# Kernel optimization log

Hardware: AMD Instinct MI355X
Metric: run time of the kernel (lower is better)

## Reference

```python
import jax, jax.numpy as jnp
import numpy as np

D_MODEL = 256; N_LAYERS = 4; INPUT_LEN = 15
D_INNER = 512; D_STATE = 16; D_CONV = 4; DT_RANK = 16
BATCH = 4; SEQ = 2048; EPS = 1e-5

def _ln(x, w, b):
    m = jnp.mean(x, -1, keepdims=True)
    v = jnp.var(x, -1, keepdims=True)
    return (x - m) * jax.lax.rsqrt(v + EPS) * w + b

def _silu(x):
    return x * jax.nn.sigmoid(x)

def _mixer(h, inW, cw, cb, xpW, dtW, dtb, A_log, Dp, opW):
    # h: [B,L,d_model]
    xz = h @ inW.T                      # [B,L,2*D_INNER]
    xh, z = jnp.split(xz, 2, axis=-1)
    # causal depthwise conv1d
    xc = jnp.transpose(xh, (0, 2, 1))   # [B,D,L]
    xc = jax.lax.conv_general_dilated(xc, cw, (1,), [(D_CONV - 1, 0)],
                                      feature_group_count=D_INNER,
                                      dimension_numbers=('NCH', 'OIH', 'NCH'))
    xc = xc + cb[None, :, None]
    xh = _silu(jnp.transpose(xc, (0, 2, 1)))  # [B,L,D]
    dbl = xh @ xpW.T                    # [B,L,DT_RANK+2N]
    dt = dbl[..., :DT_RANK]
    Bm = dbl[..., DT_RANK:DT_RANK + D_STATE]
    C = dbl[..., DT_RANK + D_STATE:]
    dt = jax.nn.softplus(dt @ dtW.T + dtb)    # [B,L,D]
    A = -jnp.exp(A_log)                       # [D,N]
    dA = jnp.exp(dt[..., None] * A)           # [B,L,D,N]
    dBu = dt[..., None] * Bm[:, :, None, :] * xh[..., None]  # [B,L,D,N]
    def step(hst, inp):
        dA_t, dBu_t, C_t = inp
        hst = dA_t * hst + dBu_t
        y = jnp.einsum('bdn,bn->bd', hst, C_t)
        return hst, y
    h0 = jnp.zeros((xh.shape[0], D_INNER, D_STATE), xh.dtype)
    _, ys = jax.lax.scan(step, h0, (jnp.transpose(dA, (1, 0, 2, 3)),
                                    jnp.transpose(dBu, (1, 0, 2, 3)),
                                    jnp.transpose(C, (1, 0, 2))))
    y = jnp.transpose(ys, (1, 0, 2)) + Dp * xh
    y = y * _silu(z)
    return y @ opW.T

def setup_inputs():
    key = jax.random.key(0)
    ks = jax.random.split(key, 8)
    s = 0.02
    return {
        'x_src': jax.random.normal(ks[0], (BATCH, SEQ, INPUT_LEN), jnp.float32),
        'single_eval_pos': 1024,
        'in_W': jax.random.normal(ks[1], (D_MODEL, INPUT_LEN)) * s,
        'norm_w': jnp.ones((N_LAYERS, D_MODEL)),
        'norm_b': jnp.zeros((N_LAYERS, D_MODEL)),
        'inproj_W': jax.random.normal(ks[2], (N_LAYERS, 2 * D_INNER, D_MODEL)) * s,
        'conv_w': jax.random.normal(ks[3], (N_LAYERS, D_INNER, 1, D_CONV)) * 0.2,
        'conv_b': jnp.zeros((N_LAYERS, D_INNER)),
        'xproj_W': jax.random.normal(ks[4], (N_LAYERS, DT_RANK + 2 * D_STATE, D_INNER)) * s,
        'dtproj_W': jax.random.normal(ks[5], (N_LAYERS, D_INNER, DT_RANK)) * 0.1,
        'dtproj_b': jnp.log(jnp.expm1(jnp.full((N_LAYERS, D_INNER), 0.01))),
        'A_log': jnp.log(jnp.broadcast_to(jnp.arange(1, D_STATE + 1, dtype=jnp.float32), (N_LAYERS, D_INNER, D_STATE)) + 0.0),
        'D_param': jnp.ones((N_LAYERS, D_INNER)),
        'outproj_W': jax.random.normal(ks[6], (N_LAYERS, D_MODEL, D_INNER)) * s,
        'out_W': jax.random.normal(ks[7], (1, D_MODEL)) * s,
    }

def reference(x_src, single_eval_pos, in_W, norm_w, norm_b, inproj_W, conv_w, conv_b, xproj_W, dtproj_W, dtproj_b, A_log, D_param, outproj_W, out_W):
    h = x_src @ in_W.T                  # [B,L,d_model]
    res = None
    for i in range(N_LAYERS):
        res = h if res is None else h + res
        hn = _ln(res, norm_w[i], norm_b[i])
        h = _mixer(hn, inproj_W[i], conv_w[i], conv_b[i], xproj_W[i],
                   dtproj_W[i], dtproj_b[i], A_log[i], D_param[i], outproj_W[i])
    # backbone returns hidden_states directly (norm_f defined but not applied)
    return h @ out_W.T                  # [B,L,1]
```

## Files before the change

### kernel.cpp

```cpp
#include <hip/hip_runtime.h>

#define B_   4
#define T_   2048
#define BT_  8192
#define INL  15
#define DM   256
#define DI   512
#define DX   1024
#define DS_  16
#define DR_  16
#define NO_  48
#define NL   4
#define NC_  128
#define LCH  16

typedef short bf16x8 __attribute__((ext_vector_type(8)));
typedef float f32x4  __attribute__((ext_vector_type(4)));

__device__ __forceinline__ float sigmoidf_(float x){ return 1.f/(1.f+__expf(-x)); }

__device__ __forceinline__ unsigned short f2bf(float x){
    union { float f; unsigned u; } v; v.f = x;
    unsigned r = (v.u + 0x7FFFu + ((v.u >> 16) & 1u)) >> 16;
    return (unsigned short)r;
}
__device__ __forceinline__ float bf2f(unsigned short h){
    union { unsigned u; float f; } v; v.u = ((unsigned)h) << 16;
    return v.f;
}

__device__ __forceinline__ void ld16(const float* __restrict__ p, float* v){
    const float4* q = (const float4*)p;
    float4 x0=q[0],x1=q[1],x2=q[2],x3=q[3];
    v[0]=x0.x; v[1]=x0.y; v[2]=x0.z; v[3]=x0.w;
    v[4]=x1.x; v[5]=x1.y; v[6]=x1.z; v[7]=x1.w;
    v[8]=x2.x; v[9]=x2.y; v[10]=x2.z; v[11]=x2.w;
    v[12]=x3.x; v[13]=x3.y; v[14]=x3.z; v[15]=x3.w;
}
__device__ __forceinline__ void st16(float* __restrict__ p, const float* v){
    float4* q = (float4*)p;
    q[0] = make_float4(v[0],v[1],v[2],v[3]);
    q[1] = make_float4(v[4],v[5],v[6],v[7]);
    q[2] = make_float4(v[8],v[9],v[10],v[11]);
    q[3] = make_float4(v[12],v[13],v[14],v[15]);
}

__global__ void k_cvtW(const float* __restrict__ W, unsigned short* __restrict__ hi,
                       unsigned short* __restrict__ lo, int n4){
    int g = blockIdx.x*256 + threadIdx.x;
    if(g >= n4) return;
    float4 v = ((const float4*)W)[g];
    ushort4 h, l;
    h.x = f2bf(v.x); l.x = f2bf(v.x - bf2f(h.x));
    h.y = f2bf(v.y); l.y = f2bf(v.y - bf2f(h.y));
    h.z = f2bf(v.z); l.z = f2bf(v.z - bf2f(h.z));
    h.w = f2bf(v.w); l.w = f2bf(v.w - bf2f(h.w));
    ((ushort4*)hi)[g] = h;
    ((ushort4*)lo)[g] = l;
}

__global__ void k_ingemm(const float* __restrict__ x, const float* __restrict__ W,
                         float* __restrict__ h){
    int g  = blockIdx.x*256 + threadIdx.x;
    int bt = g >> 8, m = g & 255;
    const float* xr = x + bt*INL;
    const float* wr = W + m*INL;
    float acc = 0.f;
#pragma unroll
    for(int k=0;k<INL;k++) acc += xr[k]*wr[k];
    h[g] = acc;
}

__global__ void k_resln(const float* __restrict__ h, float* __restrict__ res,
                        unsigned short* __restrict__ hnhi, unsigned short* __restrict__ hnlo,
                        const float* __restrict__ w, const float* __restrict__ b, int addRes){
    int wv = threadIdx.x >> 6, lane = threadIdx.x & 63;
    int bt = blockIdx.x*4 + wv;
    float4 v = ((const float4*)(h + (size_t)bt*DM))[lane];
    if(addRes){
        float4 r = ((const float4*)(res + (size_t)bt*DM))[lane];
        v.x+=r.x; v.y+=r.y; v.z+=r.z; v.w+=r.w;
    }
    ((float4*)(res + (size_t)bt*DM))[lane] = v;
    float s  = v.x+v.y+v.z+v.w;
    float ss = v.x*v.x+v.y*v.y+v.z*v.z+v.w*v.w;
#pragma unroll
    for(int m=1;m<64;m<<=1){ s += __shfl_xor(s,m); ss += __shfl_xor(ss,m); }
    float mean = s*(1.f/DM);
    float var  = ss*(1.f/DM) - mean*mean;
    float inv  = rsqrtf(var + 1e-5f);
    float4 wt = ((const float4*)w)[lane];
    float4 bs = ((const float4*)b)[lane];
    float4 o;
    o.x = (v.x-mean)*inv*wt.x + bs.x;
    o.y = (v.y-mean)*inv*wt.y + bs.y;
    o.z = (v.z-mean)*inv*wt.z + bs.z;
    o.w = (v.w-mean)*inv*wt.w + bs.w;
    ushort4 hh, ll;
    hh.x = f2bf(o.x); ll.x = f2bf(o.x - bf2f(hh.x));
    hh.y = f2bf(o.y); ll.y = f2bf(o.y - bf2f(hh.y));
    hh.z = f2bf(o.z); ll.z = f2bf(o.z - bf2f(hh.z));
    hh.w = f2bf(o.w); ll.w = f2bf(o.w - bf2f(hh.w));
    ((ushort4*)(hnhi + (size_t)bt*DM))[lane] = hh;
    ((ushort4*)(hnlo + (size_t)bt*DM))[lane] = ll;
}

template<int BM,int BN>
__global__ void __launch_bounds__(256) k_gemm_bf3(
    const unsigned short* __restrict__ Ahi, const unsigned short* __restrict__ Alo,
    const unsigned short* __restrict__ Bhi, const unsigned short* __restrict__ Blo,
    float* __restrict__ C, int M, int N, int K)
{
    constexpr int LDP = 40;
    constexpr int WM = BM/2, WN = BN/2;
    constexpr int MI_ = WM/16, NI_ = WN/16;
    __shared__ unsigned short sAh[BM*LDP], sAl[BM*LDP], sBh[BN*LDP], sBl[BN*LDP];
    int tid  = threadIdx.x;
    int wave = tid >> 6, lane = tid & 63;
    int wm0  = (wave >> 1) * WM, wn0 = (wave & 1) * WN;
    int m0   = blockIdx.y * BM, n0 = blockIdx.x * BN;
    int lr   = lane & 15;
    int kq   = (lane >> 4) * 8;
    int quad4 = (lane >> 4) * 4;

    f32x4 acc[MI_][NI_];
#pragma unroll
    for(int i=0;i<MI_;i++)
#pragma unroll
        for(int j=0;j<NI_;j++) acc[i][j] = (f32x4){0.f,0.f,0.f,0.f};

    for(int k0=0;k0<K;k0+=32){
#pragma unroll
        for(int i=tid;i<BM*4;i+=256){
            int r = i>>2, cg = (i&3)*8;
            size_t go = (size_t)(m0+r)*K + k0 + cg;
            *(float4*)(&sAh[r*LDP + cg]) = *(const float4*)(Ahi + go);
            *(float4*)(&sAl[r*LDP + cg]) = *(const float4*)(Alo + go);
        }
#pragma unroll
        for(int i=tid;i<BN*4;i+=256){
            int r = i>>2, cg = (i&3)*8;
            size_t go = (size_t)(n0+r)*K + k0 + cg;
            *(float4*)(&sBh[r*LDP + cg]) = *(const float4*)(Bhi + go);
            *(float4*)(&sBl[r*LDP + cg]) = *(const float4*)(Blo + go);
        }
        __syncthreads();
        bf16x8 ah[MI_], al[MI_], bh[NI_], bl[NI_];
#pragma unroll
        for(int mi=0;mi<MI_;mi++){
            int ro = (wm0 + mi*16 + lr)*LDP + kq;
            ah[mi] = *(const bf16x8*)(&sAh[ro]);
            al[mi] = *(const bf16x8*)(&sAl[ro]);
        }
#pragma unroll
        for(int ni=0;ni<NI_;ni++){
            int ro = (wn0 + ni*16 + lr)*LDP + kq;
            bh[ni] = *(const bf16x8*)(&sBh[ro]);
            bl[ni] = *(const bf16x8*)(&sBl[ro]);
        }
#pragma unroll
        for(int mi=0;mi<MI_;mi++)
#pragma unroll
            for(int ni=0;ni<NI_;ni++){
                acc[mi][ni] = __builtin_amdgcn_mfma_f32_16x16x32_bf16(ah[mi], bh[ni], acc[mi][ni], 0,0,0);
                acc[mi][ni] = __builtin_amdgcn_mfma_f32_16x16x32_bf16(ah[mi], bl[ni], acc[mi][ni], 0,0,0);
                acc[mi][ni] = __builtin_amdgcn_mfma_f32_16x16x32_bf16(al[mi], bh[ni], acc[mi][ni], 0,0,0);
            }
        __syncthreads();
    }
#pragma unroll
    for(int mi=0;mi<MI_;mi++)
#pragma unroll
        for(int ni=0;ni<NI_;ni++){
            int col = n0 + wn0 + ni*16 + lr;
#pragma unroll
            for(int r=0;r<4;r++){
                int row = m0 + wm0 + mi*16 + quad4 + r;
                C[(size_t)row*N + col] = acc[mi][ni][r];
            }
        }
}

__global__ void __launch_bounds__(512) k_convxp(
    const float* __restrict__ xz, const float* __restrict__ cw, const float* __restrict__ cb,
    const unsigned short* __restrict__ Bhi, const unsigned short* __restrict__ Blo,
    const float* __restrict__ dtW, const float* __restrict__ dtbias,
    const float* __restrict__ A_log,
    float* __restrict__ xh, float* __restrict__ bc, float* __restrict__ dtO,
    float* __restrict__ S, float* __restrict__ sdt)
{
    __shared__ unsigned short sAh[16*520], sAl[16*520];
    __shared__ float sbc[16*36];
    __shared__ float dls[16*17];

    int tid = threadIdx.x;
    int wave = tid >> 6, lane = tid & 63;
    int lr = lane & 15, kq = (lane>>4)*8, quad4 = (lane>>4)*4;
    int m0 = blockIdx.x * LCH;
    int d  = tid;

    float xv[19];
    {
        int rbase = m0 - 3;
        bool mask0 = ((m0 & (T_-1)) == 0);
#pragma unroll
        for(int j=0;j<19;j++)
            xv[j] = (mask0 && j<3) ? 0.f : xz[(size_t)(rbase+j)*DX + d];
    }
    float4 w4 = *(const float4*)(cw + d*4);
    float bias = cb[d];
    float xhreg[16];
#pragma unroll
    for(int t=0;t<16;t++){
        float a = bias + w4.x*xv[t] + w4.y*xv[t+1] + w4.z*xv[t+2] + w4.w*xv[t+3];
        float v = a * sigmoidf_(a);
        xhreg[t] = v;
        xh[(size_t)(m0+t)*DI + d] = v;
        unsigned short hh = f2bf(v);
        sAh[t*520 + d] = hh;
        sAl[t*520 + d] = f2bf(v - bf2f(hh));
    }
    float wr_[16]; ld16(dtW + (size_t)d*16, wr_);
    float a_[16];  ld16(A_log + (size_t)d*16, a_);
#pragma unroll
    for(int n=0;n<16;n++) a_[n] = -__expf(a_[n]);
    float bsv = dtbias[d];
    __syncthreads();

    f32x4 acc = {0.f,0.f,0.f,0.f};
    if(wave < 3){
#pragma unroll 4
        for(int ks=0;ks<16;ks++){
            int ao = lr*520 + ks*32 + kq;
            bf16x8 ah = *(const bf16x8*)(&sAh[ao]);
            bf16x8 al = *(const bf16x8*)(&sAl[ao]);
            size_t wo = (size_t)(wave*16 + lr)*DI + ks*32 + kq;
            bf16x8 bh = *(const bf16x8*)(Bhi + wo);
            bf16x8 bl = *(const bf16x8*)(Blo + wo);
            acc = __builtin_amdgcn_mfma_f32_16x16x32_bf16(ah, bh, acc, 0,0,0);
            acc = __builtin_amdgcn_mfma_f32_16x16x32_bf16(ah, bl, acc, 0,0,0);
            acc = __builtin_amdgcn_mfma_f32_16x16x32_bf16(al, bh, acc, 0,0,0);
        }
        if(wave == 0){
#pragma unroll
            for(int r=0;r<4;r++) dls[(quad4+r)*17 + lr] = acc[r];
        } else if(wave == 1){
#pragma unroll
            for(int r=0;r<4;r++){
                sbc[(quad4+r)*36 + lr] = acc[r];
                bc[(size_t)(m0+quad4+r)*32 + lr] = acc[r];
            }
        } else {
#pragma unroll
            for(int r=0;r<4;r++){
                sbc[(quad4+r)*36 + 16 + lr] = acc[r];
                bc[(size_t)(m0+quad4+r)*32 + 16 + lr] = acc[r];
            }
        }
    }
    __syncthreads();

    float dtreg[16];
#pragma unroll
    for(int t=0;t<16;t++){
        float acc2 = bsv;
#pragma unroll
        for(int r=0;r<16;r++) acc2 += dls[t*17 + r]*wr_[r];
        float sp = fmaxf(acc2,0.f) + log1pf(__expf(-fabsf(acc2)));
        dtreg[t] = sp;
        dtO[(size_t)(m0+t)*DI + d] = sp;
    }
    float st_[16];
#pragma unroll
    for(int n=0;n<16;n++) st_[n] = 0.f;
    float sd = 0.f;
#pragma unroll 4
    for(int t=0;t<16;t++){
        float dtv = dtreg[t];
        float dx  = dtv*xhreg[t];
        sd += dtv;
        float bv[16]; ld16(&sbc[t*36], bv);
#pragma unroll
        for(int n=0;n<16;n++) st_[n] = __expf(dtv*a_[n])*st_[n] + dx*bv[n];
    }
    int b = m0 >> 11, c = (m0 >> 4) & (NC_-1);
    st16(S + (((size_t)b*NC_ + c)*DI + d)*16, st_);
    sdt[((size_t)b*NC_ + c)*DI + d] = sd;
}

__global__ void k_scan2(const float* __restrict__ S, const float* __restrict__ sdt,
                        const float* __restrict__ A_log, float* __restrict__ Hinit){
    int g = blockIdx.x*256 + threadIdx.x;
    int b = g >> 13;
    int dn = g & 8191;
    int d = dn >> 4;
    float a = -__expf(A_log[dn]);
    float H = 0.f;
    for(int c=0;c<NC_;c++){
        size_t o = ((size_t)(b*NC_ + c))*8192 + dn;
        Hinit[o] = H;
        float sd = sdt[(size_t)(b*NC_ + c)*DI + d];
        H = __expf(sd*a)*H + S[o];
    }
}

__global__ void __launch_bounds__(512) k_scan3o(
    const float* __restrict__ dt, const float* __restrict__ xh, const float* __restrict__ xz,
    const float* __restrict__ bc, const float* __restrict__ A_log, const float* __restrict__ Dpar,
    const float* __restrict__ Hinit, const unsigned short* __restrict__ Whi,
    const unsigned short* __restrict__ Wlo, float* __restrict__ hOut)
{
    __shared__ unsigned short sYh[16*540], sYl[16*540];
    __shared__ float sbc[16*36];
    int tid = threadIdx.x;
    int c = blockIdx.x, b = blockIdx.y;
    int m0 = b*T_ + c*LCH;
    if(tid < 128){
        int t = tid >> 3, s = tid & 7;
        *(float4*)(&sbc[t*36 + s*4]) = *(const float4*)(bc + (size_t)(m0+t)*32 + s*4);
    }
    __syncthreads();
    {
        int d = tid;
        float a_[16]; ld16(A_log + (size_t)d*16, a_);
#pragma unroll
        for(int n=0;n<16;n++) a_[n] = -__expf(a_[n]);
        float st_[16]; ld16(Hinit + (((size_t)b*NC_ + c)*DI + d)*16, st_);
        float Dp = Dpar[d];
#pragma unroll 4
        for(int t=0;t<LCH;t++){
            int bt = m0 + t;
            float dtv = dt[(size_t)bt*DI + d];
            float xhv = xh[(size_t)bt*DI + d];
            float bv[16]; ld16(&sbc[t*36], bv);
            float cv[16]; ld16(&sbc[t*36 + 16], cv);
            float dx = dtv*xhv;
            float y = 0.f;
#pragma unroll
            for(int n=0;n<16;n++){
                st_[n] = __expf(dtv*a_[n])*st_[n] + dx*bv[n];
                y += st_[n]*cv[n];
            }
            float zv = xz[(size_t)bt*DX + DI + d];
            y += Dp*xhv;
            y = y * zv * sigmoidf_(zv);
            unsigned short hh = f2bf(y);
            sYh[t*540 + d] = hh;
            sYl[t*540 + d] = f2bf(y - bf2f(hh));
        }
    }
    __syncthreads();
    int wave = tid >> 6, lane = tid & 63;
    int lr = lane & 15, kq = (lane>>4)*8, quad4 = (lane>>4)*4;
    f32x4 acc[2];
    acc[0] = (f32x4){0.f,0.f,0.f,0.f};
    acc[1] = (f32x4){0.f,0.f,0.f,0.f};
#pragma unroll 4
    for(int ks=0;ks<16;ks++){
        int ao = lr*540 + ks*32 + kq;
        bf16x8 ah = *(const bf16x8*)(&sYh[ao]);
        bf16x8 al = *(const bf16x8*)(&sYl[ao]);
#pragma unroll
        for(int nj=0;nj<2;nj++){
            int n = (wave*2 + nj)*16 + lr;
            size_t wo = (size_t)n*DI + ks*32 + kq;
            bf16x8 bh = *(const bf16x8*)(Whi + wo);
            bf16x8 bl = *(const bf16x8*)(Wlo + wo);
            acc[nj] = __builtin_amdgcn_mfma_f32_16x16x32_bf16(ah, bh, acc[nj], 0,0,0);
            acc[nj] = __builtin_amdgcn_mfma_f32_16x16x32_bf16(ah, bl, acc[nj], 0,0,0);
            acc[nj] = __builtin_amdgcn_mfma_f32_16x16x32_bf16(al, bh, acc[nj], 0,0,0);
        }
    }
#pragma unroll
    for(int nj=0;nj<2;nj++){
        int col = (wave*2 + nj)*16 + lr;
#pragma unroll
        for(int r=0;r<4;r++){
            int row = m0 + quad4 + r;
            hOut[(size_t)row*DM + col] = acc[nj][r];
        }
    }
}

__global__ void k_outw(const float* __restrict__ h, const float* __restrict__ ow,
                       float* __restrict__ out){
    int wv = threadIdx.x >> 6, lane = threadIdx.x & 63;
    int bt = blockIdx.x*4 + wv;
    float4 v = ((const float4*)(h + (size_t)bt*DM))[lane];
    float4 w = ((const float4*)ow)[lane];
    float s = v.x*w.x + v.y*w.y + v.z*w.z + v.w*w.w;
#pragma unroll
    for(int m=1;m<64;m<<=1) s += __shfl_xor(s,m);
    if(lane==0) out[bt] = s;
}

extern "C" void kernel_launch(void* const* d_in, const int* in_sizes, int n_in,
                              void* d_out, int out_size, void* d_ws, size_t ws_size,
                              hipStream_t stream){
    const float* x_src    = (const float*)d_in[0];
    const float* in_W     = (const float*)d_in[2];
    const float* norm_w   = (const float*)d_in[3];
    const float* norm_b   = (const float*)d_in[4];
    const float* inproj_W = (const float*)d_in[5];
    const float* conv_w   = (const float*)d_in[6];
    const float* conv_b   = (const float*)d_in[7];
    const float* xproj_W  = (const float*)d_in[8];
    const float* dtproj_W = (const float*)d_in[9];
    const float* dtproj_b = (const float*)d_in[10];
    const float* A_log    = (const float*)d_in[11];
    const float* D_param  = (const float*)d_in[12];
    const float* outproj_W= (const float*)d_in[13];
    const float* out_W    = (const float*)d_in[14];

    float* ws  = (float*)d_ws;
    float* h    = ws;
    float* res  = h    + (size_t)BT_*DM;
    float* xz   = res  + (size_t)BT_*DM;
    float* xh   = xz   + (size_t)BT_*DX;
    float* bcb  = xh   + (size_t)BT_*DI;
    float* dtb  = bcb  + (size_t)BT_*32;
    float* sdtb = dtb  + (size_t)BT_*DI;
    float* Sbuf = sdtb + (size_t)B_*NC_*DI;
    float* Hbuf = Sbuf + (size_t)B_*NC_*DI*DS_;
    unsigned short* us = (unsigned short*)(Hbuf + (size_t)B_*NC_*DI*DS_);
    unsigned short* WhiIn  = us;
    unsigned short* WloIn  = WhiIn  + (size_t)NL*DX*DM;
    unsigned short* WhiOut = WloIn  + (size_t)NL*DX*DM;
    unsigned short* WloOut = WhiOut + (size_t)NL*DM*DI;
    unsigned short* WhiXp  = WloOut + (size_t)NL*DM*DI;
    unsigned short* WloXp  = WhiXp  + (size_t)NL*NO_*DI;
    unsigned short* hnhi   = WloXp  + (size_t)NL*NO_*DI;
    unsigned short* hnlo   = hnhi   + (size_t)BT_*DM;

    k_cvtW<<<(NL*DX*DM/4 + 255)/256, 256, 0, stream>>>(inproj_W,  WhiIn,  WloIn,  NL*DX*DM/4);
    k_cvtW<<<(NL*DM*DI/4 + 255)/256, 256, 0, stream>>>(outproj_W, WhiOut, WloOut, NL*DM*DI/4);
    k_cvtW<<<(NL*NO_*DI/4 + 255)/256, 256, 0, stream>>>(xproj_W, WhiXp, WloXp, NL*NO_*DI/4);
    k_ingemm<<<BT_*DM/256, 256, 0, stream>>>(x_src, in_W, h);
    for(int i=0;i<NL;i++){
        k_resln<<<BT_/4, 256, 0, stream>>>(h, res, hnhi, hnlo, norm_w + i*DM, norm_b + i*DM, i>0 ? 1 : 0);
        k_gemm_bf3<128,128><<<dim3(DX/128, BT_/128), 256, 0, stream>>>(
            hnhi, hnlo, WhiIn + (size_t)i*DX*DM, WloIn + (size_t)i*DX*DM, xz, BT_, DX, DM);
        k_convxp<<<BT_/LCH, 512, 0, stream>>>(xz, conv_w + i*DI*4, conv_b + i*DI,
            WhiXp + (size_t)i*NO_*DI, WloXp + (size_t)i*NO_*DI,
            dtproj_W + (size_t)i*DI*DR_, dtproj_b + i*DI, A_log + (size_t)i*DI*DS_,
            xh, bcb, dtb, Sbuf, sdtb);
        k_scan2<<<B_*DI*DS_/256, 256, 0, stream>>>(Sbuf, sdtb, A_log + (size_t)i*DI*DS_, Hbuf);
        k_scan3o<<<dim3(NC_, B_), 512, 0, stream>>>(dtb, xh, xz, bcb, A_log + (size_t)i*DI*DS_,
            D_param + i*DI, Hbuf, WhiOut + (size_t)i*DM*DI, WloOut + (size_t)i*DM*DI, h);
    }
    k_outw<<<BT_/4, 256, 0, stream>>>(h, out_W, (float*)d_out);
}
```

Before: 627.8 us.

## Split out-projection into tiled GEMM fused with residual add and layernorm

The scan kernel no longer computes the out-projection. It writes packed hi/lo bf16 outputs to a buffer instead. A new 64-row tiled MFMA kernel stages the out-projection weights in shared memory, reusing them across 64 rows rather than reloading them from global memory for every 16-row chunk. The same kernel fuses the residual add and the next layer's layernorm, which removes the separate resln launch for layers after the first. The cost is an extra round trip of the Y buffer through global memory and one more kernel launch per layer.

```diff
diff --git a/kernel.cpp b/kernel.cpp
--- a/kernel.cpp
+++ b/kernel.cpp
@@ -304,13 +304,11 @@
     }
 }
 
-__global__ void __launch_bounds__(512) k_scan3o(
+__global__ void __launch_bounds__(512) k_scan3(
     const float* __restrict__ dt, const float* __restrict__ xh, const float* __restrict__ xz,
     const float* __restrict__ bc, const float* __restrict__ A_log, const float* __restrict__ Dpar,
-    const float* __restrict__ Hinit, const unsigned short* __restrict__ Whi,
-    const unsigned short* __restrict__ Wlo, float* __restrict__ hOut)
+    const float* __restrict__ Hinit, unsigned* __restrict__ Y)
 {
-    __shared__ unsigned short sYh[16*540], sYl[16*540];
     __shared__ float sbc[16*36];
     int tid = threadIdx.x;
     int c = blockIdx.x, b = blockIdx.y;
@@ -320,65 +318,152 @@
         *(float4*)(&sbc[t*36 + s*4]) = *(const float4*)(bc + (size_t)(m0+t)*32 + s*4);
     }
     __syncthreads();
-    {
-        int d = tid;
-        float a_[16]; ld16(A_log + (size_t)d*16, a_);
-#pragma unroll
-        for(int n=0;n<16;n++) a_[n] = -__expf(a_[n]);
-        float st_[16]; ld16(Hinit + (((size_t)b*NC_ + c)*DI + d)*16, st_);
-        float Dp = Dpar[d];
+    int d = tid;
+    float a_[16]; ld16(A_log + (size_t)d*16, a_);
+#pragma unroll
+    for(int n=0;n<16;n++) a_[n] = -__expf(a_[n]);
+    float st_[16]; ld16(Hinit + (((size_t)b*NC_ + c)*DI + d)*16, st_);
+    float Dp = Dpar[d];
 #pragma unroll 4
-        for(int t=0;t<LCH;t++){
-            int bt = m0 + t;
-            float dtv = dt[(size_t)bt*DI + d];
-            float xhv = xh[(size_t)bt*DI + d];
-            float bv[16]; ld16(&sbc[t*36], bv);
-            float cv[16]; ld16(&sbc[t*36 + 16], cv);
-            float dx = dtv*xhv;
-            float y = 0.f;
-#pragma unroll
-            for(int n=0;n<16;n++){
-                st_[n] = __expf(dtv*a_[n])*st_[n] + dx*bv[n];
-                y += st_[n]*cv[n];
+    for(int t=0;t<LCH;t++){
+        int bt = m0 + t;
+        float dtv = dt[(size_t)bt*DI + d];
+        float xhv = xh[(size_t)bt*DI + d];
+        float bv[16]; ld16(&sbc[t*36], bv);
+        float cv[16]; ld16(&sbc[t*36 + 16], cv);
+        float dx = dtv*xhv;
+        float y = 0.f;
+#pragma unroll
+        for(int n=0;n<16;n++){
+            st_[n] = __expf(dtv*a_[n])*st_[n] + dx*bv[n];
+            y += st_[n]*cv[n];
+        }
+        float zv = xz[(size_t)bt*DX + DI + d];
+        y += Dp*xhv;
+        y = y * zv * sigmoidf_(zv);
+        unsigned short hh = f2bf(y);
+        unsigned short ll = f2bf(y - bf2f(hh));
+        Y[(size_t)bt*DI + d] = (unsigned)hh | ((unsigned)ll << 16);
+    }
+}
+
+__global__ void __launch_bounds__(256) k_outln(
+    const unsigned* __restrict__ Y, const unsigned short* __restrict__ Bhi,
+    const unsigned short* __restrict__ Blo, float* __restrict__ res,
+    const float* __restrict__ nw, const float* __restrict__ nb,
+    unsigned short* __restrict__ hnhi, unsigned short* __restrict__ hnlo,
+    float* __restrict__ hOut, int last)
+{
+    __shared__ __align__(16) char smem[66560];
+    unsigned short* sAh = (unsigned short*)smem;
+    unsigned short* sAl = sAh + 64*40;
+    unsigned short* sBh = sAl + 64*40;
+    unsigned short* sBl = sBh + 256*40;
+    float* sC = (float*)smem;
+
+    int tid = threadIdx.x;
+    int wave = tid >> 6, lane = tid & 63;
+    int wm0 = (wave >> 1)*32, wn0 = (wave & 1)*128;
+    int m0 = blockIdx.x*64;
+    int lr = lane & 15, kq = (lane>>4)*8, quad4 = (lane>>4)*4;
+
+    f32x4 acc[2][8];
+#pragma unroll
+    for(int i=0;i<2;i++)
+#pragma unroll
+        for(int j=0;j<8;j++) acc[i][j] = (f32x4){0.f,0.f,0.f,0.f};
+
+    for(int k0=0;k0<DI;k0+=32){
+        {
+            int r = tid>>2, s = tid&3;
+            const uint4* yp = (const uint4*)(Y + (size_t)(m0+r)*DI + k0 + s*8);
+            uint4 p0 = yp[0], p1 = yp[1];
+            union { bf16x8 v; unsigned short u[8]; } H, L;
+            H.u[0]=(unsigned short)p0.x; L.u[0]=(unsigned short)(p0.x>>16);
+            H.u[1]=(unsigned short)p0.y; L.u[1]=(unsigned short)(p0.y>>16);
+            H.u[2]=(unsigned short)p0.z; L.u[2]=(unsigned short)(p0.z>>16);
+            H.u[3]=(unsigned short)p0.w; L.u[3]=(unsigned short)(p0.w>>16);
+            H.u[4]=(unsigned short)p1.x; L.u[4]=(unsigned short)(p1.x>>16);
+            H.u[5]=(unsigned short)p1.y; L.u[5]=(unsigned short)(p1.y>>16);
+            H.u[6]=(unsigned short)p1.z; L.u[6]=(unsigned short)(p1.z>>16);
+            H.u[7]=(unsigned short)p1.w; L.u[7]=(unsigned short)(p1.w>>16);
+            *(bf16x8*)(&sAh[r*40 + s*8]) = H.v;
+            *(bf16x8*)(&sAl[r*40 + s*8]) = L.v;
+        }
+#pragma unroll
+        for(int i=tid;i<1024;i+=256){
+            int r = i>>2, s = i&3;
+            size_t go = (size_t)r*DI + k0 + s*8;
+            *(float4*)(&sBh[r*40 + s*8]) = *(const float4*)(Bhi + go);
+            *(float4*)(&sBl[r*40 + s*8]) = *(const float4*)(Blo + go);
+        }
+        __syncthreads();
+        bf16x8 ah[2], al[2];
+#pragma unroll
+        for(int mi=0;mi<2;mi++){
+            int ro = (wm0 + mi*16 + lr)*40 + kq;
+            ah[mi] = *(const bf16x8*)(&sAh[ro]);
+            al[mi] = *(const bf16x8*)(&sAl[ro]);
+        }
+#pragma unroll
+        for(int ni=0;ni<8;ni++){
+            int ro = (wn0 + ni*16 + lr)*40 + kq;
+            bf16x8 bh = *(const bf16x8*)(&sBh[ro]);
+            bf16x8 bl = *(const bf16x8*)(&sBl[ro]);
+#pragma unroll
+            for(int mi=0;mi<2;mi++){
+                acc[mi][ni] = __builtin_amdgcn_mfma_f32_16x16x32_bf16(ah[mi], bh, acc[mi][ni], 0,0,0);
+                acc[mi][ni] = __builtin_amdgcn_mfma_f32_16x16x32_bf16(ah[mi], bl, acc[mi][ni], 0,0,0);
+                acc[mi][ni] = __builtin_amdgcn_mfma_f32_16x16x32_bf16(al[mi], bh, acc[mi][ni], 0,0,0);
             }
-            float zv = xz[(size_t)bt*DX + DI + d];
-            y += Dp*xhv;
-            y = y * zv * sigmoidf_(zv);
-            unsigned short hh = f2bf(y);
-            sYh[t*540 + d] = hh;
-            sYl[t*540 + d] = f2bf(y - bf2f(hh));
-        }
-    }
+        }
+        __syncthreads();
+    }
+#pragma unroll
+    for(int mi=0;mi<2;mi++)
+#pragma unroll
+        for(int ni=0;ni<8;ni++){
+            int col = wn0 + ni*16 + lr;
+#pragma unroll
+            for(int r=0;r<4;r++)
+                sC[(wm0 + mi*16 + quad4 + r)*260 + col] = acc[mi][ni][r];
+        }
     __syncthreads();
-    int wave = tid >> 6, lane = tid & 63;
-    int lr = lane & 15, kq = (lane>>4)*8, quad4 = (lane>>4)*4;
-    f32x4 acc[2];
-    acc[0] = (f32x4){0.f,0.f,0.f,0.f};
-    acc[1] = (f32x4){0.f,0.f,0.f,0.f};
-#pragma unroll 4
-    for(int ks=0;ks<16;ks++){
-        int ao = lr*540 + ks*32 + kq;
-        bf16x8 ah = *(const bf16x8*)(&sYh[ao]);
-        bf16x8 al = *(const bf16x8*)(&sYl[ao]);
-#pragma unroll
-        for(int nj=0;nj<2;nj++){
-            int n = (wave*2 + nj)*16 + lr;
-            size_t wo = (size_t)n*DI + ks*32 + kq;
-            bf16x8 bh = *(const bf16x8*)(Whi + wo);
-            bf16x8 bl = *(const bf16x8*)(Wlo + wo);
-            acc[nj] = __builtin_amdgcn_mfma_f32_16x16x32_bf16(ah, bh, acc[nj], 0,0,0);
-            acc[nj] = __builtin_amdgcn_mfma_f32_16x16x32_bf16(ah, bl, acc[nj], 0,0,0);
-            acc[nj] = __builtin_amdgcn_mfma_f32_16x16x32_bf16(al, bh, acc[nj], 0,0,0);
-        }
-    }
-#pragma unroll
-    for(int nj=0;nj<2;nj++){
-        int col = (wave*2 + nj)*16 + lr;
-#pragma unroll
-        for(int r=0;r<4;r++){
-            int row = m0 + quad4 + r;
-            hOut[(size_t)row*DM + col] = acc[nj][r];
-        }
+    float4 wt, bs;
+    if(!last){
+        wt = ((const float4*)nw)[lane];
+        bs = ((const float4*)nb)[lane];
+    }
+    for(int j=0;j<16;j++){
+        int row = wave*16 + j;
+        int gr  = m0 + row;
+        float4 cv = *(float4*)(&sC[row*260 + lane*4]);
+        if(last){
+            ((float4*)(hOut + (size_t)gr*DM))[lane] = cv;
+            continue;
+        }
+        float4 rv = ((const float4*)(res + (size_t)gr*DM))[lane];
+        cv.x+=rv.x; cv.y+=rv.y; cv.z+=rv.z; cv.w+=rv.w;
+        ((float4*)(res + (size_t)gr*DM))[lane] = cv;
+        float s  = cv.x+cv.y+cv.z+cv.w;
+        float ss = cv.x*cv.x+cv.y*cv.y+cv.z*cv.z+cv.w*cv.w;
+#pragma unroll
+        for(int m=1;m<64;m<<=1){ s += __shfl_xor(s,m); ss += __shfl_xor(ss,m); }
+        float mean = s*(1.f/DM);
+        float var  = ss*(1.f/DM) - mean*mean;
+        float inv  = rsqrtf(var + 1e-5f);
+        float4 o;
+        o.x = (cv.x-mean)*inv*wt.x + bs.x;
+        o.y = (cv.y-mean)*inv*wt.y + bs.y;
+        o.z = (cv.z-mean)*inv*wt.z + bs.z;
+        o.w = (cv.w-mean)*inv*wt.w + bs.w;
+        ushort4 hh, ll;
+        hh.x = f2bf(o.x); ll.x = f2bf(o.x - bf2f(hh.x));
+        hh.y = f2bf(o.y); ll.y = f2bf(o.y - bf2f(hh.y));
+        hh.z = f2bf(o.z); ll.z = f2bf(o.z - bf2f(hh.z));
+        hh.w = f2bf(o.w); ll.w = f2bf(o.w - bf2f(hh.w));
+        ((ushort4*)(hnhi + (size_t)gr*DM))[lane] = hh;
+        ((ushort4*)(hnlo + (size_t)gr*DM))[lane] = ll;
     }
 }
 
@@ -431,13 +516,14 @@
     unsigned short* WloXp  = WhiXp  + (size_t)NL*NO_*DI;
     unsigned short* hnhi   = WloXp  + (size_t)NL*NO_*DI;
     unsigned short* hnlo   = hnhi   + (size_t)BT_*DM;
+    unsigned*       ybuf   = (unsigned*)(hnlo + (size_t)BT_*DM);
 
     k_cvtW<<<(NL*DX*DM/4 + 255)/256, 256, 0, stream>>>(inproj_W,  WhiIn,  WloIn,  NL*DX*DM/4);
     k_cvtW<<<(NL*DM*DI/4 + 255)/256, 256, 0, stream>>>(outproj_W, WhiOut, WloOut, NL*DM*DI/4);
     k_cvtW<<<(NL*NO_*DI/4 + 255)/256, 256, 0, stream>>>(xproj_W, WhiXp, WloXp, NL*NO_*DI/4);
     k_ingemm<<<BT_*DM/256, 256, 0, stream>>>(x_src, in_W, h);
+    k_resln<<<BT_/4, 256, 0, stream>>>(h, res, hnhi, hnlo, norm_w, norm_b, 0);
     for(int i=0;i<NL;i++){
-        k_resln<<<BT_/4, 256, 0, stream>>>(h, res, hnhi, hnlo, norm_w + i*DM, norm_b + i*DM, i>0 ? 1 : 0);
         k_gemm_bf3<128,128><<<dim3(DX/128, BT_/128), 256, 0, stream>>>(
             hnhi, hnlo, WhiIn + (size_t)i*DX*DM, WloIn + (size_t)i*DX*DM, xz, BT_, DX, DM);
         k_convxp<<<BT_/LCH, 512, 0, stream>>>(xz, conv_w + i*DI*4, conv_b + i*DI,
@@ -445,8 +531,13 @@
             dtproj_W + (size_t)i*DI*DR_, dtproj_b + i*DI, A_log + (size_t)i*DI*DS_,
             xh, bcb, dtb, Sbuf, sdtb);
         k_scan2<<<B_*DI*DS_/256, 256, 0, stream>>>(Sbuf, sdtb, A_log + (size_t)i*DI*DS_, Hbuf);
-        k_scan3o<<<dim3(NC_, B_), 512, 0, stream>>>(dtb, xh, xz, bcb, A_log + (size_t)i*DI*DS_,
-            D_param + i*DI, Hbuf, WhiOut + (size_t)i*DM*DI, WloOut + (size_t)i*DM*DI, h);
+        k_scan3<<<dim3(NC_, B_), 512, 0, stream>>>(dtb, xh, xz, bcb, A_log + (size_t)i*DI*DS_,
+            D_param + i*DI, Hbuf, ybuf);
+        int last = (i == NL-1) ? 1 : 0;
+        const float* nw = last ? norm_w : (norm_w + (i+1)*DM);
+        const float* nb = last ? norm_b : (norm_b + (i+1)*DM);
+        k_outln<<<BT_/64, 256, 0, stream>>>(ybuf, WhiOut + (size_t)i*DM*DI, WloOut + (size_t)i*DM*DI,
+            res, nw, nb, hnhi, hnlo, h, last);
     }
     k_outw<<<BT_/4, 256, 0, stream>>>(h, out_W, (float*)d_out);
 }
```

Result: slower. 672.9 us (+7.2%).
